# Kernel tuning notes

Measured on AMD Instinct MI355X. Metric: run time of the kernel, lower is better.

## Reference

```python
import jax, jax.numpy as jnp
import numpy as np

BIN_SIZE = 256  # init arg bin_size
K = 16          # init arg k


def setup_inputs() -> dict:
    key = jax.random.key(0)
    k1, k2 = jax.random.split(key)
    x = jax.random.normal(k1, (2, 8192, 256), dtype=jnp.float32)          # (B, N, D)
    codebook = jax.random.normal(k2, (256, 32), dtype=jnp.float32)        # (D, max_num_bins//2)
    return {"x": x, "codebook": codebook}


def reference(x, codebook):
    B, N, D = x.shape
    n_bins = N // BIN_SIZE
    # LSH binning: project onto random hyperplanes, argmax over [proj, -proj]
    mul = jnp.matmul(x, codebook[:, : n_bins // 2])          # (B, N, n_bins//2)
    cmul = jnp.concatenate([mul, -mul], axis=-1)             # (B, N, n_bins)
    bin_idx = jnp.argmax(cmul, axis=-1)                      # (B, N)
    # stable sort points by bin id -> equal-size bins (matches torch.argsort)
    bins_split = jnp.argsort(bin_idx, axis=-1).reshape(B, n_bins, BIN_SIZE)
    # gather points into bins
    pts = jnp.take_along_axis(x, bins_split.reshape(B, N, 1), axis=1)
    pts = pts.reshape(B, n_bins, BIN_SIZE, D)
    # per-bin dense similarity + sigmoid
    dm = jax.nn.sigmoid(jnp.einsum('bnid,bnjd->bnik'.replace('k', 'j'), pts, pts))  # (B, n_bins, BIN, BIN)
    vals, inds = jax.lax.top_k(dm, K)                        # (B, n_bins, BIN, K)
    # map local bin indices back to global point indices
    flat_split = bins_split.reshape(B, N)
    bin_off = jnp.arange(n_bins, dtype=inds.dtype)[None, :, None, None] * BIN_SIZE
    gdst = jnp.take_along_axis(flat_split, (bin_off + inds).reshape(B, -1), axis=1)
    gdst = gdst.reshape(B, n_bins, BIN_SIZE, K)
    gsrc = jnp.broadcast_to(bins_split[..., None], vals.shape)
    bidx = jnp.broadcast_to(jnp.arange(B)[:, None, None, None], vals.shape)
    # coalesced sparse adjacency, represented densely (duplicates summed like coalesce())
    out = jnp.zeros((B, N, N), x.dtype).at[bidx, gsrc, gdst].add(vals)
    return out
```

## Files before the change

### kernel.cpp

```cpp
#include <hip/hip_runtime.h>
#include <math.h>

#define BB    2
#define NN    8192
#define DD    256
#define NBINS 32
#define BINSZ 256
#define NPROJ 16
#define TOPK  16
#define NPTS  (BB * NN)

__global__ __launch_bounds__(64) void k_bins(const float* __restrict__ x,
                                             const float* __restrict__ cb,
                                             int* __restrict__ bin_idx) {
    __shared__ float cbt[DD][NPROJ];
    const int t = threadIdx.x;
    for (int q = t; q < DD * NPROJ; q += 64) {
        int d = q >> 4, j = q & 15;
        cbt[d][j] = cb[d * 32 + j];
    }
    __syncthreads();

    const int p = blockIdx.x * 64 + t;
    const float* xr = x + (size_t)p * DD;

    double a[NPROJ];
#pragma unroll
    for (int j = 0; j < NPROJ; ++j) a[j] = 0.0;

    for (int d0 = 0; d0 < DD; d0 += 4) {
        float4 xv = *(const float4*)(xr + d0);
        float xs[4] = {xv.x, xv.y, xv.z, xv.w};
#pragma unroll
        for (int dd = 0; dd < 4; ++dd) {
            double xd = (double)xs[dd];
#pragma unroll
            for (int j = 0; j < NPROJ; ++j)
                a[j] = fma((double)cbt[d0 + dd][j], xd, a[j]);
        }
    }

    float bv = -INFINITY; int bj = 0;
#pragma unroll
    for (int j = 0; j < NPROJ; ++j) {
        float m = (float)a[j];
        if (m > bv) { bv = m; bj = j; }
    }
#pragma unroll
    for (int j = 0; j < NPROJ; ++j) {
        float m = -(float)a[j];
        if (m > bv) { bv = m; bj = j + NPROJ; }
    }
    bin_idx[p] = bj;
}

__global__ __launch_bounds__(256) void k_sort(const int* __restrict__ bin_idx,
                                              int* __restrict__ order) {
    __shared__ int c[NBINS][256];
    __shared__ int base[NBINS];
    const int t = threadIdx.x;
    const int b = blockIdx.x;
    const int* bi = bin_idx + b * NN;

    for (int j = 0; j < NBINS; ++j) c[j][t] = 0;
    __syncthreads();

    const int i0 = t * 32;
    for (int i = 0; i < 32; ++i) c[bi[i0 + i]][t]++;
    __syncthreads();

    if (t < NBINS) {
        int s = 0;
        for (int q = 0; q < 256; ++q) s += c[t][q];
        base[t] = s;
    }
    __syncthreads();
    if (t == 0) {
        int run = 0;
        for (int j = 0; j < NBINS; ++j) { int tmp = base[j]; base[j] = run; run += tmp; }
    }
    __syncthreads();
    if (t < NBINS) {
        int run = base[t];
        for (int q = 0; q < 256; ++q) { int tmp = c[t][q]; c[t][q] = run; run += tmp; }
    }
    __syncthreads();

    int* ob = order + b * NN;
    for (int i = 0; i < 32; ++i) {
        int gi = i0 + i;
        int bb = bi[gi];
        int pos = c[bb][t]++;
        ob[pos] = gi;
    }
}

#define RT 32
__global__ __launch_bounds__(256) void k_sim(const float* __restrict__ x,
                                             const int* __restrict__ order,
                                             float* __restrict__ out) {
    __shared__ int    idx[BINSZ];
    __shared__ double Ad[RT][33];
    __shared__ float  S[RT][BINSZ + 1];

    const int t   = threadIdx.x;
    const int bid = blockIdx.x;
    const int b   = bid >> 8;
    const int bin = (bid >> 3) & 31;
    const int r0  = (bid & 7) * RT;

    idx[t] = order[b * NN + bin * BINSZ + t];
    __syncthreads();

    const float* xb = x + (size_t)b * NN * DD;
    const float* xc = xb + (size_t)idx[t] * DD;

    double acc[RT];
#pragma unroll
    for (int r = 0; r < RT; ++r) acc[r] = 0.0;

#pragma unroll 1
    for (int k0 = 0; k0 < DD; k0 += 32) {
        float bcol[32];
#pragma unroll
        for (int q = 0; q < 8; ++q) {
            float4 v = *(const float4*)(xc + k0 + q * 4);
            bcol[q * 4 + 0] = v.x; bcol[q * 4 + 1] = v.y;
            bcol[q * 4 + 2] = v.z; bcol[q * 4 + 3] = v.w;
        }
        {
            int r  = t >> 3;
            int qg = t & 7;
            const float* ar = xb + (size_t)idx[r0 + r] * DD + k0 + qg * 4;
            float4 v = *(const float4*)ar;
            Ad[r][qg * 4 + 0] = (double)v.x;
            Ad[r][qg * 4 + 1] = (double)v.y;
            Ad[r][qg * 4 + 2] = (double)v.z;
            Ad[r][qg * 4 + 3] = (double)v.w;
        }
        __syncthreads();
#pragma unroll
        for (int dd = 0; dd < 32; ++dd) {
            double bd = (double)bcol[dd];
#pragma unroll
            for (int r = 0; r < RT; ++r)
                acc[r] = fma(Ad[r][dd], bd, acc[r]);
        }
        __syncthreads();
    }

#pragma unroll
    for (int r = 0; r < RT; ++r) {
        float s32 = (float)acc[r];
        S[r][t] = 1.0f / (1.0f + expf(-s32));
    }
    __syncthreads();

    if (t < RT) {
        float tv[TOPK]; int ti[TOPK];
#pragma unroll
        for (int q = 0; q < TOPK; ++q) { tv[q] = -INFINITY; ti[q] = 0; }
        for (int cc = 0; cc < BINSZ; ++cc) {
            float v = S[t][cc];
            if (v > tv[TOPK - 1]) {
                tv[TOPK - 1] = v; ti[TOPK - 1] = cc;
#pragma unroll
                for (int q = TOPK - 1; q > 0; --q) {
                    if (tv[q] > tv[q - 1]) {
                        float fv = tv[q]; tv[q] = tv[q - 1]; tv[q - 1] = fv;
                        int   fi = ti[q]; ti[q] = ti[q - 1]; ti[q - 1] = fi;
                    }
                }
            }
        }
        const int gsrc = idx[r0 + t];
        float* orow = out + ((size_t)b * NN + gsrc) * NN;
#pragma unroll
        for (int q = 0; q < TOPK; ++q)
            orow[idx[ti[q]]] = tv[q];
    }
}

extern "C" void kernel_launch(void* const* d_in, const int* in_sizes, int n_in,
                              void* d_out, int out_size, void* d_ws, size_t ws_size,
                              hipStream_t stream) {
    const float* x  = (const float*)d_in[0];
    const float* cb = (const float*)d_in[1];
    float* out      = (float*)d_out;

    int* bin_idx = (int*)d_ws;
    int* order   = bin_idx + NPTS;

    hipMemsetAsync(d_out, 0, (size_t)out_size * sizeof(float), stream);

    k_bins<<<NPTS / 64, 64, 0, stream>>>(x, cb, bin_idx);
    k_sort<<<BB, 256, 0, stream>>>(bin_idx, order);
    k_sim<<<BB * NBINS * 8, 256, 0, stream>>>(x, order, out);
}
```

Baseline: 789.3 us.

## Fuse output zeroing into similarity kernel and spread top-k scatter across threads

Removes the separate memset of the full B×N×N output. Each similarity block now zeroes the rows it owns with float4 stores before computing. The top-k results are staged in shared memory so all 256 threads share the scatter writes instead of 32. It also vectorises the codebook load in the binning kernel and adds a min-blocks-per-CU launch bound to the similarity kernel. Correctness depends on each output row being owned by exactly one block, which holds because every point lands in exactly one bin slot.

```diff
diff --git a/kernel.cpp b/kernel.cpp
--- a/kernel.cpp
+++ b/kernel.cpp
@@ -15,9 +15,11 @@
                                              int* __restrict__ bin_idx) {
     __shared__ float cbt[DD][NPROJ];
     const int t = threadIdx.x;
-    for (int q = t; q < DD * NPROJ; q += 64) {
-        int d = q >> 4, j = q & 15;
-        cbt[d][j] = cb[d * 32 + j];
+    for (int q = t; q < DD * 4; q += 64) {
+        int d = q >> 2, j4 = q & 3;
+        float4 v = *(const float4*)(cb + d * 32 + j4 * 4);
+        cbt[d][j4 * 4 + 0] = v.x; cbt[d][j4 * 4 + 1] = v.y;
+        cbt[d][j4 * 4 + 2] = v.z; cbt[d][j4 * 4 + 3] = v.w;
     }
     __syncthreads();
 
@@ -96,12 +98,14 @@
 }
 
 #define RT 32
-__global__ __launch_bounds__(256) void k_sim(const float* __restrict__ x,
-                                             const int* __restrict__ order,
-                                             float* __restrict__ out) {
+__global__ __launch_bounds__(256, 2) void k_sim(const float* __restrict__ x,
+                                                const int* __restrict__ order,
+                                                float* __restrict__ out) {
     __shared__ int    idx[BINSZ];
     __shared__ double Ad[RT][33];
     __shared__ float  S[RT][BINSZ + 1];
+    __shared__ float  tvs[RT][TOPK];
+    __shared__ int    tds[RT][TOPK];
 
     const int t   = threadIdx.x;
     const int bid = blockIdx.x;
@@ -111,6 +115,17 @@
 
     idx[t] = order[b * NN + bin * BINSZ + t];
     __syncthreads();
+
+    {
+        const float4 z = make_float4(0.f, 0.f, 0.f, 0.f);
+#pragma unroll 1
+        for (int r = 0; r < RT; ++r) {
+            float4* orow = (float4*)(out + ((size_t)b * NN + idx[r0 + r]) * NN);
+#pragma unroll
+            for (int j = 0; j < 8; ++j)
+                orow[j * 256 + t] = z;
+        }
+    }
 
     const float* xb = x + (size_t)b * NN * DD;
     const float* xc = xb + (size_t)idx[t] * DD;
@@ -173,11 +188,19 @@
                 }
             }
         }
-        const int gsrc = idx[r0 + t];
-        float* orow = out + ((size_t)b * NN + gsrc) * NN;
-#pragma unroll
-        for (int q = 0; q < TOPK; ++q)
-            orow[idx[ti[q]]] = tv[q];
+#pragma unroll
+        for (int q = 0; q < TOPK; ++q) {
+            tvs[t][q] = tv[q];
+            tds[t][q] = idx[ti[q]];
+        }
+    }
+    __syncthreads();
+
+#pragma unroll
+    for (int p = t; p < RT * TOPK; p += 256) {
+        int r = p >> 4, q = p & 15;
+        float* orow = out + ((size_t)b * NN + idx[r0 + r]) * NN;
+        orow[tds[r][q]] = tvs[r][q];
     }
 }
 
@@ -191,8 +214,6 @@
     int* bin_idx = (int*)d_ws;
     int* order   = bin_idx + NPTS;
 
-    hipMemsetAsync(d_out, 0, (size_t)out_size * sizeof(float), stream);
-
     k_bins<<<NPTS / 64, 64, 0, stream>>>(x, cb, bin_idx);
     k_sort<<<BB, 256, 0, stream>>>(bin_idx, order);
     k_sim<<<BB * NBINS * 8, 256, 0, stream>>>(x, order, out);
```

Result: slower. 815.2 us (+3.3%).
